# Kernel optimization log

Hardware: AMD Instinct MI355X
Metric: run time of the kernel (lower is better)

The kernel has to match this reference:

```python
import jax, jax.numpy as jnp
import numpy as np
import math

D = 256        # input_size == d_k == d_v (per the module: d_k = input_size)
H = 4          # n_heads
MAX_LEN = 800  # PositionalEncoding max_len
NEG = float(-(2**32) + 1)
LN_EPS = 1e-5


def _make_pe():
    pe = np.zeros((MAX_LEN, D), dtype=np.float32)
    pos = np.arange(MAX_LEN, dtype=np.float32)[:, None]
    div = np.exp(np.arange(0, D, 2, dtype=np.float32) * -(math.log(10000.0) / D))
    pe[:, 0::2] = np.sin(pos * div)
    pe[:, 1::2] = np.cos(pos * div)
    return jnp.asarray(pe)


def setup_inputs() -> dict:
    key = jax.random.key(0)
    ks = jax.random.split(key, 12)
    B, L = 32, 512

    def xavier(k, shape):
        fan_in, fan_out = shape[0], shape[1]
        std = math.sqrt(2.0 / (fan_in + fan_out))
        return jax.random.normal(k, shape, dtype=jnp.float32) * std

    return {
        "Q": jax.random.normal(ks[0], (B, L, D), dtype=jnp.float32),
        "K": jax.random.normal(ks[1], (B, L, D), dtype=jnp.float32),
        "V": jax.random.normal(ks[2], (B, L, D), dtype=jnp.float32),
        "mask": jax.random.randint(ks[3], (B, L), 0, 2).astype(jnp.bool_),
        "pe": _make_pe(),
        "W_q": xavier(ks[4], (D, H * D)),
        "W_k": xavier(ks[5], (D, H * D)),
        "W_v": xavier(ks[6], (D, H * D)),
        "W_o": xavier(ks[7], (H * D, D)),
        "w1": xavier(ks[8], (D, D)),
        "b1": jnp.zeros((D,), dtype=jnp.float32),
        "w2": xavier(ks[9], (D, D)),
        "b2": jnp.zeros((D,), dtype=jnp.float32),
        "gamma": jnp.ones((D,), dtype=jnp.float32),
        "beta": jnp.zeros((D,), dtype=jnp.float32),
    }


def _layer_norm(x, gamma, beta):
    mu = jnp.mean(x, axis=-1, keepdims=True)
    var = jnp.mean(jnp.square(x - mu), axis=-1, keepdims=True)
    return (x - mu) * jax.lax.rsqrt(var + LN_EPS) * gamma + beta


def _mha(Q, K, V, mask, W_q, W_k, W_v, W_o):
    B, Lq, _ = Q.shape
    Lk = K.shape[1]

    def split_heads(X, W, L):
        # (B, L, D) @ (D, H*D) -> (B*H, L, D)
        return (X @ W).reshape(B, L, H, D).transpose(0, 2, 1, 3).reshape(B * H, L, D)

    Qh = split_heads(Q, W_q, Lq)
    Kh = split_heads(K, W_k, Lk)
    Vh = split_heads(V, W_v, Lk)

    scale = D ** 0.5 + 1e-6
    scores = jnp.einsum('bqd,bkd->bqk', Qh, Kh) / scale  # (B*H, Lq, Lk)

    pad = jnp.broadcast_to(mask[:, None, :], (B, H, Lq)).reshape(B * H, Lq)
    pad_mask = jnp.broadcast_to(pad[:, :, None], (B * H, Lq, Lk))
    causal = jnp.triu(jnp.ones((Lq, Lk), dtype=jnp.bool_), k=1)
    full_mask = causal[None] | pad_mask
    scores = jnp.where(full_mask, NEG, scores)

    att = jax.nn.softmax(scores, axis=-1)
    Vatt = jnp.einsum('bqk,bkd->bqd', att, Vh)  # (B*H, Lq, D)
    Vatt = Vatt.reshape(B, H, Lq, D).transpose(0, 2, 1, 3).reshape(B, Lq, H * D)
    return Vatt @ W_o


def reference(Q, K, V, mask, pe, W_q, W_k, W_v, W_o, w1, b1, w2, b2, gamma, beta):
    Lq, Lk, Lv = Q.shape[1], K.shape[1], V.shape[1]
    Qp = Q + pe[None, :Lq]
    Kp = K + pe[None, :Lk]
    Vp = V + pe[None, :Lv]

    Vatt = _mha(Qp, Kp, Vp, mask, W_q, W_k, W_v, W_o)
    X = _layer_norm(Qp + Vatt, gamma, beta)
    ffn = jax.nn.relu(X @ w1.T + b1) @ w2.T + b2
    return _layer_norm(ffn + X, gamma, beta)
```

## Files before the change

kernel.cpp:

```cpp
#include <hip/hip_runtime.h>
#include <stdint.h>

#define SEQ   512
#define DM    256
#define NB    32
#define NH    4
#define HD    (NH * DM)
#define PE_MASK (SEQ * DM - 1)
#define NEGV  (-4294967295.0f)

typedef __attribute__((ext_vector_type(8))) short short8;
typedef __attribute__((ext_vector_type(4))) float f32x4;

#if defined(__has_builtin)
#if __has_builtin(__builtin_amdgcn_global_load_lds)
#define HAS_ASYNC 1
#endif
#endif
#ifndef HAS_ASYNC
#define HAS_ASYNC 0
#endif

__device__ __forceinline__ float b2f(unsigned short u) {
    return __uint_as_float(((uint32_t)u) << 16);
}
__device__ __forceinline__ unsigned short f2b(float f) {
    uint32_t u = __float_as_uint(f);
    u += 0x7fffu + ((u >> 16) & 1u);
    return (unsigned short)(u >> 16);
}

__global__ __launch_bounds__(256) void mask_canon(
    const unsigned char* __restrict__ raw, int* __restrict__ canon)
{
    __shared__ int enc_byte, enc_odd;
    int tid = threadIdx.x;
    if (tid == 0) { enc_byte = 0; enc_odd = 0; }
    __syncthreads();
    if (tid < 255 && raw[tid * 4 + 1]) atomicOr(&enc_byte, 1);
    if (tid < 128 && ((const int*)raw)[tid * 2 + 1]) atomicOr(&enc_odd, 1);
    __syncthreads();
    int i = blockIdx.x * 256 + tid;
    int v;
    if (enc_byte)      v = (raw[i] != 0);
    else if (enc_odd)  v = (((const int*)raw)[i] != 0);
    else               v = ((((const int*)raw)[i * 2] | ((const int*)raw)[i * 2 + 1]) != 0);
    canon[i] = v;
}

__global__ __launch_bounds__(256) void addpe3(
    const float* __restrict__ Q, const float* __restrict__ K,
    const float* __restrict__ V, const float* __restrict__ pe,
    unsigned short* __restrict__ Qp, unsigned short* __restrict__ Kp,
    unsigned short* __restrict__ Vp)
{
    int blk = blockIdx.x;
    int seg = blk >> 12;
    const float* X = (seg == 0) ? Q : (seg == 1) ? K : V;
    unsigned short* O = (seg == 0) ? Qp : (seg == 1) ? Kp : Vp;
    long i = (long)((blk & 4095) * 256 + threadIdx.x) * 4;
    float4 x = *reinterpret_cast<const float4*>(X + i);
    float4 p = *reinterpret_cast<const float4*>(pe + (i & PE_MASK));
    ushort4 o;
    o.x = f2b(x.x + p.x); o.y = f2b(x.y + p.y);
    o.z = f2b(x.z + p.z); o.w = f2b(x.w + p.w);
    *reinterpret_cast<ushort4*>(O + i) = o;
}

__global__ __launch_bounds__(256) void conv2(
    const float* __restrict__ w1, const float* __restrict__ w2,
    unsigned short* __restrict__ o1, unsigned short* __restrict__ o2)
{
    int blk = blockIdx.x;
    const float* in = (blk < 64) ? w1 : w2;
    unsigned short* out = (blk < 64) ? o1 : o2;
    long i = (long)((blk & 63) * 256 + threadIdx.x) * 4;
    float4 x = *reinterpret_cast<const float4*>(in + i);
    ushort4 o;
    o.x = f2b(x.x); o.y = f2b(x.y); o.z = f2b(x.z); o.w = f2b(x.w);
    *reinterpret_cast<ushort4*>(out + i) = o;
}

__global__ __launch_bounds__(256) void transpose_f2b3(
    const float* __restrict__ in0, const float* __restrict__ in1,
    const float* __restrict__ in2, unsigned short* __restrict__ out,
    int ldin, int ldout, long outStride)
{
    int z = blockIdx.z;
    const float* in = (z == 0) ? in0 : (z == 1) ? in1 : in2;
    unsigned short* op = out + z * outStride;
    __shared__ unsigned short tile[32][33];
    int r0 = blockIdx.y * 32, c0 = blockIdx.x * 32;
    int i = threadIdx.x >> 3;
    int j = (threadIdx.x & 7) * 4;
    float4 v = *reinterpret_cast<const float4*>(in + (long)(r0 + i) * ldin + c0 + j);
    tile[i][j + 0] = f2b(v.x); tile[i][j + 1] = f2b(v.y);
    tile[i][j + 2] = f2b(v.z); tile[i][j + 3] = f2b(v.w);
    __syncthreads();
    ushort4 w;
    w.x = tile[j + 0][i]; w.y = tile[j + 1][i]; w.z = tile[j + 2][i]; w.w = tile[j + 3][i];
    *reinterpret_cast<ushort4*>(op + (long)(c0 + i) * ldout + r0 + j) = w;
}

__global__ __launch_bounds__(256) void transpose_f2b(
    const float* __restrict__ in, unsigned short* __restrict__ out,
    int ldin, int ldout)
{
    __shared__ unsigned short tile[32][33];
    int r0 = blockIdx.y * 32, c0 = blockIdx.x * 32;
    int i = threadIdx.x >> 3;
    int j = (threadIdx.x & 7) * 4;
    float4 v = *reinterpret_cast<const float4*>(in + (long)(r0 + i) * ldin + c0 + j);
    tile[i][j + 0] = f2b(v.x); tile[i][j + 1] = f2b(v.y);
    tile[i][j + 2] = f2b(v.z); tile[i][j + 3] = f2b(v.w);
    __syncthreads();
    ushort4 w;
    w.x = tile[j + 0][i]; w.y = tile[j + 1][i]; w.z = tile[j + 2][i]; w.w = tile[j + 3][i];
    *reinterpret_cast<ushort4*>(out + (long)(c0 + i) * ldout + r0 + j) = w;
}

__global__ __launch_bounds__(256) void transpose_bf16(
    const unsigned short* __restrict__ in, unsigned short* __restrict__ out,
    int ldin, int ldout, long sInB, long sInH, long sOutB, long sOutH, int Hdiv)
{
    int z = blockIdx.z; int b = z / Hdiv; int h = z % Hdiv;
    const unsigned short* ip = in + b * sInB + h * sInH;
    unsigned short* op = out + b * sOutB + h * sOutH;
    __shared__ unsigned short tile[32][33];
    int r0 = blockIdx.y * 32, c0 = blockIdx.x * 32;
    int i = threadIdx.x >> 3;
    int j = (threadIdx.x & 7) * 4;
    ushort4 v = *reinterpret_cast<const ushort4*>(ip + (long)(r0 + i) * ldin + c0 + j);
    tile[i][j + 0] = v.x; tile[i][j + 1] = v.y; tile[i][j + 2] = v.z; tile[i][j + 3] = v.w;
    __syncthreads();
    ushort4 w;
    w.x = tile[j + 0][i]; w.y = tile[j + 1][i]; w.z = tile[j + 2][i]; w.w = tile[j + 3][i];
    *reinterpret_cast<ushort4*>(op + (long)(c0 + i) * ldout + r0 + j) = w;
}

template<bool BIAS, bool RELU, bool OUTBF16>
__global__ __launch_bounds__(256) void gemm_bt(
    const unsigned short* __restrict__ A, int lda,
    const unsigned short* __restrict__ B, int ldb,
    void* __restrict__ Cv, int ldc,
    const float* __restrict__ bias, float scale, int K, int Hdiv,
    long sAb, long sAh, long sAz,
    long sBb, long sBh, long sBz,
    long sCb, long sCh, long sCz)
{
    const int m0 = blockIdx.y * 128;
    const int n0 = blockIdx.x * 128;
    int z  = blockIdx.z;
    int bb = z / Hdiv, hh = z % Hdiv;
    const unsigned short* Ab = A + bb * sAb + hh * sAh + (long)z * sAz;
    const unsigned short* Bb = B + bb * sBb + hh * sBh + (long)z * sBz;
    long coff = bb * sCb + hh * sCh + (long)z * sCz;

    __shared__ unsigned short As[128 * 32];
    __shared__ unsigned short Bs[128 * 32];

    const int tid  = threadIdx.x;
    const int lane = tid & 63;
    const int wave = tid >> 6;
    const int wm   = (wave >> 1) * 64;
    const int wn   = (wave & 1) * 64;
    const int lm   = lane & 15;
    const int kq   = (lane >> 4) * 8;

    f32x4 acc[4][4] = {};

    for (int k0 = 0; k0 < K; k0 += 32) {
#pragma unroll
        for (int it = 0; it < 2; ++it) {
            int id = tid + it * 256;
            int r  = id >> 2;
            int c8 = (id & 3) * 8;
            const unsigned short* gA = Ab + (long)(m0 + r) * lda + k0 + c8;
            const unsigned short* gB = Bb + (long)(n0 + r) * ldb + k0 + c8;
#if HAS_ASYNC
            unsigned short* lA = &As[(size_t)(it * 256 + wave * 64) * 8];
            unsigned short* lB = &Bs[(size_t)(it * 256 + wave * 64) * 8];
            __builtin_amdgcn_global_load_lds(
                (const __attribute__((address_space(1))) void*)gA,
                (__attribute__((address_space(3))) void*)lA, 16, 0, 0);
            __builtin_amdgcn_global_load_lds(
                (const __attribute__((address_space(1))) void*)gB,
                (__attribute__((address_space(3))) void*)lB, 16, 0, 0);
#else
            *reinterpret_cast<uint4*>(&As[(size_t)id * 8]) =
                *reinterpret_cast<const uint4*>(gA);
            *reinterpret_cast<uint4*>(&Bs[(size_t)id * 8]) =
                *reinterpret_cast<const uint4*>(gB);
#endif
        }
        __syncthreads();

        short8 af[4], bfr[4];
#pragma unroll
        for (int i = 0; i < 4; ++i)
            af[i] = *reinterpret_cast<const short8*>(&As[(wm + i * 16 + lm) * 32 + kq]);
#pragma unroll
        for (int j = 0; j < 4; ++j)
            bfr[j] = *reinterpret_cast<const short8*>(&Bs[(wn + j * 16 + lm) * 32 + kq]);
#pragma unroll
        for (int i = 0; i < 4; ++i)
#pragma unroll
            for (int j = 0; j < 4; ++j)
                acc[i][j] = __builtin_amdgcn_mfma_f32_16x16x32_bf16(af[i], bfr[j], acc[i][j], 0, 0, 0);
        __syncthreads();
    }

#pragma unroll
    for (int j = 0; j < 4; ++j) {
        int col  = n0 + wn + j * 16 + lm;
        float bv = 0.f;
        if (BIAS) bv = bias[col];
#pragma unroll
        for (int i = 0; i < 4; ++i) {
#pragma unroll
            for (int r = 0; r < 4; ++r) {
                int row = m0 + wm + i * 16 + (lane >> 4) * 4 + r;
                float v = acc[i][j][r] * scale + bv;
                if (RELU) v = fmaxf(v, 0.f);
                long idx = coff + (long)row * ldc + col;
                if (OUTBF16) reinterpret_cast<unsigned short*>(Cv)[idx] = f2b(v);
                else         reinterpret_cast<float*>(Cv)[idx] = v;
            }
        }
    }
}

__global__ __launch_bounds__(256) void flash_attn(
    const unsigned short* __restrict__ Qh,
    const unsigned short* __restrict__ Kh,
    const unsigned short* __restrict__ VhT,
    unsigned short* __restrict__ Vatt,
    const int* __restrict__ maskc, int bh0, float scale, int nbh)
{
    const int tid  = threadIdx.x;
    const int lane = tid & 63;
    const int wave = tid >> 6;
    const int lm   = lane & 15;
    const int qg   = lane >> 4;
    const int kq   = qg * 8;

    const int L = blockIdx.x;
    int z, qt;
    if ((nbh & 7) == 0) {
        int x = L & 7, m = L >> 3;
        qt = m & 7;
        z  = x + 8 * (m >> 3);
    } else {
        z = L % nbh; qt = L / nbh;
    }
    const int b_l = z >> 2, h = z & 3;
    const int m0  = qt * 64;
    const int wq0 = m0 + wave * 16;
    const long qkbase = (long)b_l * SEQ * HD + (long)h * DM;
    const unsigned short* Aq = Qh + qkbase;
    const unsigned short* Ak = Kh + qkbase;
    const unsigned short* Av = VhT + (long)b_l * SEQ * HD + (long)h * SEQ * DM;
    unsigned short* Ov = Vatt + qkbase;
    const int bglob = (bh0 + z) >> 2;

    __shared__ unsigned short Ks[SEQ * 32];
    __shared__ __align__(16) unsigned short Pw[4][16][40];

    f32x4 S[32] = {};
    const int NT = (m0 >> 4) + wave + 1;

    for (int kc = 0; kc < 8; ++kc) {
        for (int it = 0; it <= qt; ++it) {
            int id = tid + it * 256;
            const unsigned short* g = Ak + (long)(id >> 2) * HD + kc * 32 + (id & 3) * 8;
#if HAS_ASYNC
            unsigned short* l = &Ks[(size_t)(it * 256 + wave * 64) * 8];
            __builtin_amdgcn_global_load_lds(
                (const __attribute__((address_space(1))) void*)g,
                (__attribute__((address_space(3))) void*)l, 16, 0, 0);
#else
            *reinterpret_cast<uint4*>(&Ks[(size_t)id * 8]) =
                *reinterpret_cast<const uint4*>(g);
#endif
        }
        short8 qf = *reinterpret_cast<const short8*>(
            Aq + (long)(wq0 + lm) * HD + kc * 32 + kq);
        __syncthreads();
#pragma unroll
        for (int nt = 0; nt < 32; ++nt) {
            if (nt < NT) {
                short8 bf = *reinterpret_cast<const short8*>(&Ks[(nt * 16 + lm) * 32 + kq]);
                S[nt] = __builtin_amdgcn_mfma_f32_16x16x32_bf16(qf, bf, S[nt], 0, 0, 0);
            }
        }
        __syncthreads();
    }

    unsigned short* Vb0 = Ks;
    unsigned short* Vb1 = Ks + 8192;
#pragma unroll
    for (int it = 0; it < 4; ++it) {
        int id = tid + it * 256;
        const unsigned short* g = Av + (long)(id >> 2) * SEQ + (id & 3) * 8;
#if HAS_ASYNC
        unsigned short* l = &Vb0[(size_t)(it * 256 + wave * 64) * 8];
        __builtin_amdgcn_global_load_lds(
            (const __attribute__((address_space(1))) void*)g,
            (__attribute__((address_space(3))) void*)l, 16, 0, 0);
#else
        *reinterpret_cast<uint4*>(&Vb0[(size_t)id * 8]) =
            *reinterpret_cast<const uint4*>(g);
#endif
    }

    int   qrow[4];
    bool  rowm[4];
    float mx[4], sm[4];
#pragma unroll
    for (int r = 0; r < 4; ++r) {
        int q = wq0 + qg * 4 + r;
        qrow[r] = q;
        rowm[r] = maskc[bglob * SEQ + q] != 0;
        mx[r] = -3.4e38f;
    }
#pragma unroll
    for (int nt = 0; nt < 32; ++nt) {
        int k = nt * 16 + lm;
#pragma unroll
        for (int r = 0; r < 4; ++r) {
            float v = S[nt][r] * scale;
            if (k > qrow[r] || rowm[r]) v = NEGV;
            S[nt][r] = v;
            mx[r] = fmaxf(mx[r], v);
        }
    }
#pragma unroll
    for (int r = 0; r < 4; ++r) {
#pragma unroll
        for (int off = 8; off >= 1; off >>= 1)
            mx[r] = fmaxf(mx[r], __shfl_xor(mx[r], off));
        sm[r] = 0.f;
    }
#pragma unroll
    for (int nt = 0; nt < 32; ++nt)
#pragma unroll
        for (int r = 0; r < 4; ++r) {
            float e = __expf(S[nt][r] - mx[r]);
            S[nt][r] = e;
            sm[r] += e;
        }
#pragma unroll
    for (int r = 0; r < 4; ++r) {
#pragma unroll
        for (int off = 8; off >= 1; off >>= 1)
            sm[r] += __shfl_xor(sm[r], off);
        sm[r] = 1.0f / sm[r];
    }
#pragma unroll
    for (int nt = 0; nt < 32; ++nt)
#pragma unroll
        for (int r = 0; r < 4; ++r) S[nt][r] *= sm[r];

    f32x4 O[16] = {};
    for (int kc2 = 0; kc2 < 16; ++kc2) {
        unsigned short* Vcur = (kc2 & 1) ? Vb1 : Vb0;
        __syncthreads();
        if (kc2 < 15) {
            unsigned short* Vnext = (kc2 & 1) ? Vb0 : Vb1;
#pragma unroll
            for (int it = 0; it < 4; ++it) {
                int id = tid + it * 256;
                const unsigned short* g =
                    Av + (long)(id >> 2) * SEQ + (kc2 + 1) * 32 + (id & 3) * 8;
#if HAS_ASYNC
                unsigned short* l = &Vnext[(size_t)(it * 256 + wave * 64) * 8];
                __builtin_amdgcn_global_load_lds(
                    (const __attribute__((address_space(1))) void*)g,
                    (__attribute__((address_space(3))) void*)l, 16, 0, 0);
#else
                *reinterpret_cast<uint4*>(&Vnext[(size_t)id * 8]) =
                    *reinterpret_cast<const uint4*>(g);
#endif
            }
        }
#pragma unroll
        for (int t = 0; t < 2; ++t) {
            int nt = kc2 * 2 + t;
#pragma unroll
            for (int r = 0; r < 4; ++r)
                Pw[wave][qg * 4 + r][t * 16 + lm] = f2b(S[nt][r]);
        }
        short8 pf = *reinterpret_cast<const short8*>(&Pw[wave][lm][kq]);
#pragma unroll
        for (int nt2 = 0; nt2 < 16; ++nt2) {
            short8 vf = *reinterpret_cast<const short8*>(&Vcur[(nt2 * 16 + lm) * 32 + kq]);
            O[nt2] = __builtin_amdgcn_mfma_f32_16x16x32_bf16(pf, vf, O[nt2], 0, 0, 0);
        }
    }

#pragma unroll
    for (int nt2 = 0; nt2 < 16; ++nt2) {
#pragma unroll
        for (int r = 0; r < 4; ++r) {
            int l = wq0 + qg * 4 + r;
            Ov[(long)l * HD + nt2 * 16 + lm] = f2b(O[nt2][r]);
        }
    }
}

__global__ __launch_bounds__(256) void ln1_kernel(
    const unsigned short* __restrict__ AttO, const float* __restrict__ Q,
    const float* __restrict__ pe,
    const float* __restrict__ gamma, const float* __restrict__ beta,
    float* __restrict__ outf, unsigned short* __restrict__ outb)
{
    int row  = blockIdx.x * 4 + (threadIdx.x >> 6);
    int lane = threadIdx.x & 63;
    long base = (long)row * DM + lane * 4;
    ushort4 a = *reinterpret_cast<const ushort4*>(AttO + base);
    float4 qv = *reinterpret_cast<const float4*>(Q + base);
    float4 pv = *reinterpret_cast<const float4*>(pe + (base & PE_MASK));
    float x[4] = {b2f(a.x) + qv.x + pv.x, b2f(a.y) + qv.y + pv.y,
                  b2f(a.z) + qv.z + pv.z, b2f(a.w) + qv.w + pv.w};
    float s = x[0] + x[1] + x[2] + x[3];
#pragma unroll
    for (int off = 32; off > 0; off >>= 1) s += __shfl_xor(s, off);
    float mu = s * (1.0f / DM);
    float vs = 0.f;
#pragma unroll
    for (int t = 0; t < 4; ++t) { float d = x[t] - mu; vs += d * d; }
#pragma unroll
    for (int off = 32; off > 0; off >>= 1) vs += __shfl_xor(vs, off);
    float inv = rsqrtf(vs * (1.0f / DM) + 1e-5f);
    int d0 = lane * 4;
    float4 g = *reinterpret_cast<const float4*>(gamma + d0);
    float4 bt = *reinterpret_cast<const float4*>(beta + d0);
    float4 o;
    o.x = (x[0] - mu) * inv * g.x + bt.x;
    o.y = (x[1] - mu) * inv * g.y + bt.y;
    o.z = (x[2] - mu) * inv * g.z + bt.z;
    o.w = (x[3] - mu) * inv * g.w + bt.w;
    *reinterpret_cast<float4*>(outf + base) = o;
    ushort4 ob;
    ob.x = f2b(o.x); ob.y = f2b(o.y); ob.z = f2b(o.z); ob.w = f2b(o.w);
    *reinterpret_cast<ushort4*>(outb + base) = ob;
}

__global__ __launch_bounds__(256) void ln2_kernel(
    const float* __restrict__ F, const float* __restrict__ X,
    const float* __restrict__ gamma, const float* __restrict__ beta,
    float* __restrict__ out)
{
    int row  = blockIdx.x * 4 + (threadIdx.x >> 6);
    int lane = threadIdx.x & 63;
    long base = (long)row * DM + lane * 4;
    float4 a = *reinterpret_cast<const float4*>(F + base);
    float4 c = *reinterpret_cast<const float4*>(X + base);
    float x[4] = {a.x + c.x, a.y + c.y, a.z + c.z, a.w + c.w};
    float s = x[0] + x[1] + x[2] + x[3];
#pragma unroll
    for (int off = 32; off > 0; off >>= 1) s += __shfl_xor(s, off);
    float mu = s * (1.0f / DM);
    float vs = 0.f;
#pragma unroll
    for (int t = 0; t < 4; ++t) { float d = x[t] - mu; vs += d * d; }
#pragma unroll
    for (int off = 32; off > 0; off >>= 1) vs += __shfl_xor(vs, off);
    float inv = rsqrtf(vs * (1.0f / DM) + 1e-5f);
    int d0 = lane * 4;
    float4 g = *reinterpret_cast<const float4*>(gamma + d0);
    float4 bt = *reinterpret_cast<const float4*>(beta + d0);
    float4 o;
    o.x = (x[0] - mu) * inv * g.x + bt.x;
    o.y = (x[1] - mu) * inv * g.y + bt.y;
    o.z = (x[2] - mu) * inv * g.z + bt.z;
    o.w = (x[3] - mu) * inv * g.w + bt.w;
    *reinterpret_cast<float4*>(out + base) = o;
}

extern "C" void kernel_launch(void* const* d_in, const int* in_sizes, int n_in,
                              void* d_out, int out_size, void* d_ws, size_t ws_size,
                              hipStream_t stream)
{
    const float* Q  = (const float*)d_in[0];
    const float* Ki = (const float*)d_in[1];
    const float* Vi = (const float*)d_in[2];
    const unsigned char* mask_raw = (const unsigned char*)d_in[3];
    const float* pe = (const float*)d_in[4];
    const float* Wq = (const float*)d_in[5];
    const float* Wk = (const float*)d_in[6];
    const float* Wv = (const float*)d_in[7];
    const float* Wo = (const float*)d_in[8];
    const float* w1 = (const float*)d_in[9];
    const float* b1 = (const float*)d_in[10];
    const float* w2 = (const float*)d_in[11];
    const float* b2 = (const float*)d_in[12];
    const float* gamma = (const float*)d_in[13];
    const float* beta  = (const float*)d_in[14];
    float* out = (float*)d_out;

    const size_t MiB = 1048576;
    char* ws = (char*)d_ws;

    int CB = 1;
    for (int cb = 32; cb >= 1; cb >>= 1) {
        size_t scr_sz = (size_t)(5 * cb) * MiB;
        if (scr_sz < 24 * MiB) scr_sz = 24 * MiB;
        if ((59 * MiB + scr_sz) <= ws_size) { CB = cb; break; }
    }
    const int NCH = NB / CB;

    unsigned short* WqT  = (unsigned short*)(ws);
    unsigned short* WkT  = WqT + 262144;
    unsigned short* WvT  = WkT + 262144;
    unsigned short* WoT  = WvT + 262144;
    unsigned short* w1b  = (unsigned short*)(ws + 2 * MiB);
    unsigned short* w2b  = w1b + 65536;
    int*            maskc = (int*)(ws + 2 * MiB + 262144);
    unsigned short* Qp   = (unsigned short*)(ws + 3 * MiB);
    unsigned short* Kp   = (unsigned short*)(ws + 11 * MiB);
    unsigned short* Vp   = (unsigned short*)(ws + 19 * MiB);
    unsigned short* AttO = (unsigned short*)(ws + 27 * MiB);
    unsigned short* Xb   = (unsigned short*)(ws + 35 * MiB);
    float*          Xf   = (float*)(ws + 43 * MiB);
    char*           scr  = ws + 59 * MiB;
    unsigned short* Qh   = (unsigned short*)(scr);
    unsigned short* Kh   = (unsigned short*)(scr + (size_t)CB * MiB);
    unsigned short* Vh   = (unsigned short*)(scr + (size_t)2 * CB * MiB);
    unsigned short* VhT  = (unsigned short*)(scr + (size_t)3 * CB * MiB);
    unsigned short* Vatt = (unsigned short*)(scr + (size_t)4 * CB * MiB);
    unsigned short* H1   = (unsigned short*)(scr);
    float*          Ff   = (float*)(scr + 8 * MiB);

    const float scale = (float)(1.0 / (16.0 + 1e-6));
    const long CROWS = (long)CB * SEQ;
    const long CBELT = (long)CB * MiB / 2;

    mask_canon<<<64, 256, 0, stream>>>(mask_raw, maskc);
    transpose_f2b3<<<dim3(32, 8, 3), 256, 0, stream>>>(Wq, Wk, Wv, WqT, HD, DM, 262144);
    transpose_f2b<<<dim3(8, 32, 1), 256, 0, stream>>>(Wo, WoT, DM, HD);
    conv2<<<128, 256, 0, stream>>>(w1, w2, w1b, w2b);
    addpe3<<<12288, 256, 0, stream>>>(Q, Ki, Vi, pe, Qp, Kp, Vp);

    for (int c = 0; c < NCH; ++c) {
        const long r0   = (long)c * CROWS;
        const int  bh0  = c * CB * NH;
        const int  gy   = (int)(CROWS / 128);
        const int  nbh  = CB * NH;

        gemm_bt<false, false, true><<<dim3(8, gy, 3), 256, 0, stream>>>(
            Qp + r0 * DM, DM, WqT, DM, Qh, HD, nullptr, 1.f, DM,
            1, 4194304, 0, 0, 262144, 0, 0, CBELT, 0, 0);

        transpose_bf16<<<dim3(8, 16, CB * NH), 256, 0, stream>>>(
            Vh, VhT, HD, SEQ, (long)SEQ * HD, DM, (long)SEQ * HD, (long)SEQ * DM, NH);

        flash_attn<<<dim3(8 * nbh, 1, 1), 256, 0, stream>>>(
            Qh, Kh, VhT, Vatt, maskc, bh0, scale, nbh);

        gemm_bt<false, false, true><<<dim3(2, gy, 1), 256, 0, stream>>>(
            Vatt, HD, WoT, HD, AttO + r0 * DM, DM, nullptr, 1.f, HD,
            1, 0,0,0, 0,0,0, 0,0,0);
    }

    ln1_kernel<<<4096, 256, 0, stream>>>(AttO, Q, pe, gamma, beta, Xf, Xb);

    gemm_bt<true, true, true><<<dim3(2, 128, 1), 256, 0, stream>>>(
        Xb, DM, w1b, DM, H1, DM, b1, 1.f, DM, 1, 0,0,0, 0,0,0, 0,0,0);
    gemm_bt<true, false, false><<<dim3(2, 128, 1), 256, 0, stream>>>(
        H1, DM, w2b, DM, Ff, DM, b2, 1.f, DM, 1, 0,0,0, 0,0,0, 0,0,0);

    ln2_kernel<<<4096, 256, 0, stream>>>(Ff, Xf, gamma, beta, out);
}
```

Baseline: 387.1 us.

## Fuse positional-encoding add into QKV projection GEMM and simplify attention loads

Removes the standalone addpe3 kernel and the bf16 Qp/Kp/Vp buffers. A new proj_gemm reads fp32 Q/K/V and pe, adds them, and converts to bf16 while staging the A tile into shared memory. This avoids one full read/write pass over the activations, at the cost of re-reading fp32 A from each of the eight N-blocks. The flash_attn kernel also drops causal tile skipping and V double-buffering: it always loads and multiplies all K tiles and single-buffers V with extra barriers. That adds QK work and exposes load latency in exchange for simpler control flow.

New measurement: 397.7 us. 2.7% more time.

```diff
diff --git a/kernel.cpp b/kernel.cpp
--- a/kernel.cpp
+++ b/kernel.cpp
@@ -29,6 +29,8 @@
     u += 0x7fffu + ((u >> 16) & 1u);
     return (unsigned short)(u >> 16);
 }
+
+union U8 { unsigned short s[8]; uint4 v; };
 
 __global__ __launch_bounds__(256) void mask_canon(
     const unsigned char* __restrict__ raw, int* __restrict__ canon)
@@ -46,25 +48,6 @@
     else if (enc_odd)  v = (((const int*)raw)[i] != 0);
     else               v = ((((const int*)raw)[i * 2] | ((const int*)raw)[i * 2 + 1]) != 0);
     canon[i] = v;
-}
-
-__global__ __launch_bounds__(256) void addpe3(
-    const float* __restrict__ Q, const float* __restrict__ K,
-    const float* __restrict__ V, const float* __restrict__ pe,
-    unsigned short* __restrict__ Qp, unsigned short* __restrict__ Kp,
-    unsigned short* __restrict__ Vp)
-{
-    int blk = blockIdx.x;
-    int seg = blk >> 12;
-    const float* X = (seg == 0) ? Q : (seg == 1) ? K : V;
-    unsigned short* O = (seg == 0) ? Qp : (seg == 1) ? Kp : Vp;
-    long i = (long)((blk & 4095) * 256 + threadIdx.x) * 4;
-    float4 x = *reinterpret_cast<const float4*>(X + i);
-    float4 p = *reinterpret_cast<const float4*>(pe + (i & PE_MASK));
-    ushort4 o;
-    o.x = f2b(x.x + p.x); o.y = f2b(x.y + p.y);
-    o.z = f2b(x.z + p.z); o.w = f2b(x.w + p.w);
-    *reinterpret_cast<ushort4*>(O + i) = o;
 }
 
 __global__ __launch_bounds__(256) void conv2(
@@ -136,6 +119,94 @@
     ushort4 w;
     w.x = tile[j + 0][i]; w.y = tile[j + 1][i]; w.z = tile[j + 2][i]; w.w = tile[j + 3][i];
     *reinterpret_cast<ushort4*>(op + (long)(c0 + i) * ldout + r0 + j) = w;
+}
+
+__global__ __launch_bounds__(256) void proj_gemm(
+    const float* __restrict__ Qf, const float* __restrict__ Kf,
+    const float* __restrict__ Vf, const float* __restrict__ pe,
+    const unsigned short* __restrict__ Wt,
+    unsigned short* __restrict__ Ch,
+    long r0, long cbelt)
+{
+    const int z = blockIdx.z;
+    const float* Af = ((z == 0) ? Qf : (z == 1) ? Kf : Vf) + r0 * DM;
+    const unsigned short* Bb = Wt + (long)z * 262144;
+    unsigned short* Cb = Ch + (long)z * cbelt;
+
+    const int m0 = blockIdx.y * 128;
+    const int n0 = blockIdx.x * 128;
+
+    __shared__ unsigned short As[128 * 32];
+    __shared__ unsigned short Bs[128 * 32];
+
+    const int tid  = threadIdx.x;
+    const int lane = tid & 63;
+    const int wave = tid >> 6;
+    const int wm   = (wave >> 1) * 64;
+    const int wn   = (wave & 1) * 64;
+    const int lm   = lane & 15;
+    const int kq   = (lane >> 4) * 8;
+
+    f32x4 acc[4][4] = {};
+
+    for (int k0 = 0; k0 < DM; k0 += 32) {
+#pragma unroll
+        for (int it = 0; it < 2; ++it) {
+            int id = tid + it * 256;
+            int r  = id >> 2;
+            int c8 = (id & 3) * 8;
+            const unsigned short* gB = Bb + (long)(n0 + r) * DM + k0 + c8;
+#if HAS_ASYNC
+            unsigned short* lB = &Bs[(size_t)(it * 256 + wave * 64) * 8];
+            __builtin_amdgcn_global_load_lds(
+                (const __attribute__((address_space(1))) void*)gB,
+                (__attribute__((address_space(3))) void*)lB, 16, 0, 0);
+#else
+            *reinterpret_cast<uint4*>(&Bs[(size_t)id * 8]) =
+                *reinterpret_cast<const uint4*>(gB);
+#endif
+            long abase = (long)(m0 + r) * DM + k0 + c8;
+            float4 x0 = *reinterpret_cast<const float4*>(Af + abase);
+            float4 x1 = *reinterpret_cast<const float4*>(Af + abase + 4);
+            long pb = (long)((m0 + r) & (SEQ - 1)) * DM + k0 + c8;
+            float4 p0 = *reinterpret_cast<const float4*>(pe + pb);
+            float4 p1 = *reinterpret_cast<const float4*>(pe + pb + 4);
+            U8 u;
+            u.s[0] = f2b(x0.x + p0.x); u.s[1] = f2b(x0.y + p0.y);
+            u.s[2] = f2b(x0.z + p0.z); u.s[3] = f2b(x0.w + p0.w);
+            u.s[4] = f2b(x1.x + p1.x); u.s[5] = f2b(x1.y + p1.y);
+            u.s[6] = f2b(x1.z + p1.z); u.s[7] = f2b(x1.w + p1.w);
+            *reinterpret_cast<uint4*>(&As[(size_t)id * 8]) = u.v;
+        }
+        __syncthreads();
+
+        short8 af[4], bfr[4];
+#pragma unroll
+        for (int i = 0; i < 4; ++i)
+            af[i] = *reinterpret_cast<const short8*>(&As[(wm + i * 16 + lm) * 32 + kq]);
+#pragma unroll
+        for (int j = 0; j < 4; ++j)
+            bfr[j] = *reinterpret_cast<const short8*>(&Bs[(wn + j * 16 + lm) * 32 + kq]);
+#pragma unroll
+        for (int i = 0; i < 4; ++i)
+#pragma unroll
+            for (int j = 0; j < 4; ++j)
+                acc[i][j] = __builtin_amdgcn_mfma_f32_16x16x32_bf16(af[i], bfr[j], acc[i][j], 0, 0, 0);
+        __syncthreads();
+    }
+
+#pragma unroll
+    for (int j = 0; j < 4; ++j) {
+        int col = n0 + wn + j * 16 + lm;
+#pragma unroll
+        for (int i = 0; i < 4; ++i) {
+#pragma unroll
+            for (int r = 0; r < 4; ++r) {
+                int row = m0 + wm + i * 16 + (lane >> 4) * 4 + r;
+                Cb[(long)row * HD + col] = f2b(acc[i][j][r]);
+            }
+        }
+    }
 }
 
 template<bool BIAS, bool RELU, bool OUTBF16>
@@ -267,10 +338,10 @@
     __shared__ __align__(16) unsigned short Pw[4][16][40];
 
     f32x4 S[32] = {};
-    const int NT = (m0 >> 4) + wave + 1;
 
     for (int kc = 0; kc < 8; ++kc) {
-        for (int it = 0; it <= qt; ++it) {
+#pragma unroll
+        for (int it = 0; it < 8; ++it) {
             int id = tid + it * 256;
             const unsigned short* g = Ak + (long)(id >> 2) * HD + kc * 32 + (id & 3) * 8;
 #if HAS_ASYNC
@@ -288,29 +359,10 @@
         __syncthreads();
 #pragma unroll
         for (int nt = 0; nt < 32; ++nt) {
-            if (nt < NT) {
-                short8 bf = *reinterpret_cast<const short8*>(&Ks[(nt * 16 + lm) * 32 + kq]);
-                S[nt] = __builtin_amdgcn_mfma_f32_16x16x32_bf16(qf, bf, S[nt], 0, 0, 0);
-            }
-        }
-        __syncthreads();
-    }
-
-    unsigned short* Vb0 = Ks;
-    unsigned short* Vb1 = Ks + 8192;
-#pragma unroll
-    for (int it = 0; it < 4; ++it) {
-        int id = tid + it * 256;
-        const unsigned short* g = Av + (long)(id >> 2) * SEQ + (id & 3) * 8;
-#if HAS_ASYNC
-        unsigned short* l = &Vb0[(size_t)(it * 256 + wave * 64) * 8];
-        __builtin_amdgcn_global_load_lds(
-            (const __attribute__((address_space(1))) void*)g,
-            (__attribute__((address_space(3))) void*)l, 16, 0, 0);
-#else
-        *reinterpret_cast<uint4*>(&Vb0[(size_t)id * 8]) =
-            *reinterpret_cast<const uint4*>(g);
-#endif
+            short8 bf = *reinterpret_cast<const short8*>(&Ks[(nt * 16 + lm) * 32 + kq]);
+            S[nt] = __builtin_amdgcn_mfma_f32_16x16x32_bf16(qf, bf, S[nt], 0, 0, 0);
+        }
+        __syncthreads();
     }
 
     int   qrow[4];
@@ -362,26 +414,21 @@
         for (int r = 0; r < 4; ++r) S[nt][r] *= sm[r];
 
     f32x4 O[16] = {};
+    unsigned short* Vs = Ks;
     for (int kc2 = 0; kc2 < 16; ++kc2) {
-        unsigned short* Vcur = (kc2 & 1) ? Vb1 : Vb0;
-        __syncthreads();
-        if (kc2 < 15) {
-            unsigned short* Vnext = (kc2 & 1) ? Vb0 : Vb1;
-#pragma unroll
-            for (int it = 0; it < 4; ++it) {
-                int id = tid + it * 256;
-                const unsigned short* g =
-                    Av + (long)(id >> 2) * SEQ + (kc2 + 1) * 32 + (id & 3) * 8;
+#pragma unroll
+        for (int it = 0; it < 4; ++it) {
+            int id = tid + it * 256;
+            const unsigned short* g = Av + (long)(id >> 2) * SEQ + kc2 * 32 + (id & 3) * 8;
 #if HAS_ASYNC
-                unsigned short* l = &Vnext[(size_t)(it * 256 + wave * 64) * 8];
-                __builtin_amdgcn_global_load_lds(
-                    (const __attribute__((address_space(1))) void*)g,
-                    (__attribute__((address_space(3))) void*)l, 16, 0, 0);
+            unsigned short* l = &Vs[(size_t)(it * 256 + wave * 64) * 8];
+            __builtin_amdgcn_global_load_lds(
+                (const __attribute__((address_space(1))) void*)g,
+                (__attribute__((address_space(3))) void*)l, 16, 0, 0);
 #else
-                *reinterpret_cast<uint4*>(&Vnext[(size_t)id * 8]) =
-                    *reinterpret_cast<const uint4*>(g);
+            *reinterpret_cast<uint4*>(&Vs[(size_t)id * 8]) =
+                *reinterpret_cast<const uint4*>(g);
 #endif
-            }
         }
 #pragma unroll
         for (int t = 0; t < 2; ++t) {
@@ -390,12 +437,14 @@
             for (int r = 0; r < 4; ++r)
                 Pw[wave][qg * 4 + r][t * 16 + lm] = f2b(S[nt][r]);
         }
+        __syncthreads();
         short8 pf = *reinterpret_cast<const short8*>(&Pw[wave][lm][kq]);
 #pragma unroll
         for (int nt2 = 0; nt2 < 16; ++nt2) {
-            short8 vf = *reinterpret_cast<const short8*>(&Vcur[(nt2 * 16 + lm) * 32 + kq]);
+            short8 vf = *reinterpret_cast<const short8*>(&Vs[(nt2 * 16 + lm) * 32 + kq]);
             O[nt2] = __builtin_amdgcn_mfma_f32_16x16x32_bf16(pf, vf, O[nt2], 0, 0, 0);
         }
+        __syncthreads();
     }
 
 #pragma unroll
@@ -506,24 +555,19 @@
     for (int cb = 32; cb >= 1; cb >>= 1) {
         size_t scr_sz = (size_t)(5 * cb) * MiB;
         if (scr_sz < 24 * MiB) scr_sz = 24 * MiB;
-        if ((59 * MiB + scr_sz) <= ws_size) { CB = cb; break; }
+        if ((35 * MiB + scr_sz) <= ws_size) { CB = cb; break; }
     }
     const int NCH = NB / CB;
 
     unsigned short* WqT  = (unsigned short*)(ws);
-    unsigned short* WkT  = WqT + 262144;
-    unsigned short* WvT  = WkT + 262144;
-    unsigned short* WoT  = WvT + 262144;
+    unsigned short* WoT  = WqT + 3 * 262144;
     unsigned short* w1b  = (unsigned short*)(ws + 2 * MiB);
     unsigned short* w2b  = w1b + 65536;
     int*            maskc = (int*)(ws + 2 * MiB + 262144);
-    unsigned short* Qp   = (unsigned short*)(ws + 3 * MiB);
-    unsigned short* Kp   = (unsigned short*)(ws + 11 * MiB);
-    unsigned short* Vp   = (unsigned short*)(ws + 19 * MiB);
-    unsigned short* AttO = (unsigned short*)(ws + 27 * MiB);
-    unsigned short* Xb   = (unsigned short*)(ws + 35 * MiB);
-    float*          Xf   = (float*)(ws + 43 * MiB);
-    char*           scr  = ws + 59 * MiB;
+    unsigned short* AttO = (unsigned short*)(ws + 3 * MiB);
+    unsigned short* Xb   = (unsigned short*)(ws + 11 * MiB);
+    float*          Xf   = (float*)(ws + 19 * MiB);
+    char*           scr  = ws + 35 * MiB;
     unsigned short* Qh   = (unsigned short*)(scr);
     unsigned short* Kh   = (unsigned short*)(scr + (size_t)CB * MiB);
     unsigned short* Vh   = (unsigned short*)(scr + (size_t)2 * CB * MiB);
@@ -540,7 +584,6 @@
     transpose_f2b3<<<dim3(32, 8, 3), 256, 0, stream>>>(Wq, Wk, Wv, WqT, HD, DM, 262144);
     transpose_f2b<<<dim3(8, 32, 1), 256, 0, stream>>>(Wo, WoT, DM, HD);
     conv2<<<128, 256, 0, stream>>>(w1, w2, w1b, w2b);
-    addpe3<<<12288, 256, 0, stream>>>(Q, Ki, Vi, pe, Qp, Kp, Vp);
 
     for (int c = 0; c < NCH; ++c) {
         const long r0   = (long)c * CROWS;
@@ -548,9 +591,8 @@
         const int  gy   = (int)(CROWS / 128);
         const int  nbh  = CB * NH;
 
-        gemm_bt<false, false, true><<<dim3(8, gy, 3), 256, 0, stream>>>(
-            Qp + r0 * DM, DM, WqT, DM, Qh, HD, nullptr, 1.f, DM,
-            1, 4194304, 0, 0, 262144, 0, 0, CBELT, 0, 0);
+        proj_gemm<<<dim3(8, gy, 3), 256, 0, stream>>>(
+            Q, Ki, Vi, pe, WqT, Qh, r0, CBELT);
 
         transpose_bf16<<<dim3(8, 16, CB * NH), 256, 0, stream>>>(
             Vh, VhT, HD, SEQ, (long)SEQ * HD, DM, (long)SEQ * HD, (long)SEQ * DM, NH);
```
